# Performance work log

Measured on AMD Instinct MI355X. Metric: run time of the kernel, lower is better.

Reference implementation:

```python
import jax, jax.numpy as jnp
import numpy as np

B, S, F, H, A = 256, 128, 512, 1024, 18


def setup_inputs() -> dict:
    key = jax.random.key(0)
    ks = jax.random.split(key, 16)
    u = lambda k, shape, fan: jax.random.uniform(k, shape, jnp.float32, -1.0, 1.0) / np.sqrt(fan)
    return {
        "obs": jax.random.normal(ks[0], (B, S, F), jnp.float32),
        "hx": jax.random.normal(ks[1], (B, H), jnp.float32),
        "cx": jax.random.normal(ks[2], (B, H), jnp.float32),
        "behaviour_acts": jax.random.randint(ks[3], (B, S, 1), 0, A),
        "W1": u(ks[4], (H, F), F), "b1": u(ks[5], (H,), F),
        "W_ih": u(ks[6], (4 * H, H), H), "b_ih": u(ks[7], (4 * H,), H),
        "W_hh": u(ks[8], (4 * H, H), H), "b_hh": u(ks[9], (4 * H,), H),
        "W_v": u(ks[10], (1, H), H), "b_v": u(ks[11], (1,), H),
        "W_l": u(ks[12], (A, H), H), "b_l": u(ks[13], (A,), H),
    }


def reference(obs, hx, cx, behaviour_acts, W1, b1, W_ih, b_ih, W_hh, b_hh, W_v, b_v, W_l, b_l):
    # MLP body: [B,S,F] -> [B,S,H]
    x = jax.nn.relu(jnp.einsum("bsf,hf->bsh", obs, W1) + b1)
    # precompute input-to-gate projection for all timesteps (one big GEMM)
    xg = jnp.einsum("bsh,gh->bsg", x, W_ih) + b_ih  # [B,S,4H]

    def step(carry, xg_t):
        h, c = carry
        gates = xg_t + h @ W_hh.T + b_hh  # [B,4H], gate order i,f,g,o (torch LSTMCell)
        i, f, g, o = jnp.split(gates, 4, axis=-1)
        c = jax.nn.sigmoid(f) * c + jax.nn.sigmoid(i) * jnp.tanh(g)
        h = jax.nn.sigmoid(o) * jnp.tanh(c)
        return (h, c), h

    _, hs = jax.lax.scan(step, (hx, cx), jnp.swapaxes(xg, 0, 1))
    output = jnp.swapaxes(hs, 0, 1)  # [B,S,H]

    value = output @ W_v.T + b_v  # [B,S,1]
    logits = output @ W_l.T + b_l  # [B,S,A]
    # torch Categorical(probs=softmax(logits)) => log-prob via log_softmax
    logp = jax.nn.log_softmax(logits, axis=-1)
    acts = behaviour_acts.reshape(logits.shape[0], logits.shape[1], 1)
    log_probs = jnp.take_along_axis(logp, acts, axis=-1)  # [B,S,1]
    entropy = -jnp.sum(jnp.exp(logp) * logp, axis=-1, keepdims=True)  # [B,S,1]
    return log_probs, entropy, value
```

## Files before the change

kernel.cpp:

```cpp
#include <hip/hip_runtime.h>

#define B_ 256
#define S_ 128
#define F_ 512
#define H_ 1024
#define A_ 18
#define M_ (B_*S_)
#define G_ (4*H_)
#define CH_ 16
#define CR_ (B_*CH_)

typedef unsigned short u16;
typedef __attribute__((ext_vector_type(8))) _Float16 f16x8;
typedef __attribute__((ext_vector_type(4))) _Float16 f16x4;
typedef __attribute__((ext_vector_type(8))) short   s16x8;
typedef __attribute__((ext_vector_type(4))) float f32x4;
typedef __attribute__((ext_vector_type(4))) unsigned int u32x4;

__device__ __forceinline__ float bf2f(u16 u){
  union{unsigned int i; float f;} v; v.i=((unsigned int)u)<<16; return v.f;
}
__device__ __forceinline__ u16 f2bf(float f){
  unsigned int i=__float_as_uint(f);
  unsigned int r=(i+0x7fffu+((i>>16)&1u))>>16;
  return (u16)r;
}
__device__ __forceinline__ u16 f2h(float f){
  _Float16 h=(_Float16)f;
  union{_Float16 h; u16 u;} v; v.h=h; return v.u;
}
__device__ __forceinline__ float ldf(const void* p, size_t i, int m){
  return m ? ((const float*)p)[i] : bf2f(((const u16*)p)[i]);
}
__device__ __forceinline__ f16x8 load8_h(const void* base, size_t off, int m){
  f16x8 v;
  if(m==2) return *(const f16x8*)((const u16*)base + off);
  if(m==1){
    const float* f=(const float*)base + off;
    float4 a=*(const float4*)f; float4 b=*(const float4*)(f+4);
    v[0]=(_Float16)a.x; v[1]=(_Float16)a.y; v[2]=(_Float16)a.z; v[3]=(_Float16)a.w;
    v[4]=(_Float16)b.x; v[5]=(_Float16)b.y; v[6]=(_Float16)b.z; v[7]=(_Float16)b.w;
    return v;
  }
  s16x8 w=*(const s16x8*)((const u16*)base + off);
#pragma unroll
  for(int k=0;k<8;k++) v[k]=(_Float16)bf2f((u16)w[k]);
  return v;
}

__device__ __forceinline__ u32x4 load_c16(const void* p){
  u32x4 r;
  asm volatile("global_load_dwordx4 %0, %1, off sc0 sc1" : "=v"(r) : "v"(p));
  return r;
}
__device__ __forceinline__ void store_c2(u16* p, u16 v){
  unsigned int vv=v;
  asm volatile("global_store_short %0, %1, off sc0 sc1" :: "v"(p), "v"(vv) : "memory");
}
__device__ __forceinline__ int load_c4(const int* p){
  int r;
  asm volatile("global_load_dword %0, %1, off sc0 sc1" : "=v"(r) : "v"(p));
  return r;
}
__device__ __forceinline__ void store_c4(int* p, int v){
  asm volatile("global_store_dword %0, %1, off sc0 sc1" :: "v"(p), "v"(v) : "memory");
}

template<int ROWS, int MAP>
__device__ __forceinline__ void stage(const void* base, int mode, int lda, int k0,
                                      int rowoff, int t0, u16* lds, int tid){
  if(mode==2){
    constexpr int NI=(ROWS*8)/256;
    int wv=tid>>6, l=tid&63;
#pragma unroll
    for(int i=0;i<NI;i++){
      int s0=i*256+(wv<<6), s=s0+l;
      int r=s>>3, gc=(s&7)^(r&7);
      int p=rowoff+r, sr;
      if(MAP==0)      sr=p;
      else if(MAP==1) sr=(p&3)*H_+(p>>2);
      else            sr=(p>>4)*S_+t0+(p&15);
      const u16* src=(const u16*)base + (size_t)sr*lda + k0 + gc*8;
      u16* dst=lds + s0*8;
      __builtin_amdgcn_global_load_lds((const __attribute__((address_space(1))) unsigned int*)src,
                                       (__attribute__((address_space(3))) unsigned int*)dst,
                                       16, 0, 0);
    }
  } else {
#pragma unroll
    for(int s0=tid; s0<ROWS*8; s0+=256){
      int r=s0>>3, gc=s0&7, lc=gc^(r&7);
      int p=rowoff+r, sr;
      if(MAP==0)      sr=p;
      else if(MAP==1) sr=(p&3)*H_+(p>>2);
      else            sr=(p>>4)*S_+t0+(p&15);
      f16x8 v=load8_h(base, (size_t)sr*lda + k0 + gc*8, mode);
      *(f16x8*)(lds + r*64 + lc*8)=v;
    }
  }
}

__device__ __forceinline__ f16x8 frag_ld(const u16* lds, int r0, int kc, int lane){
  int r = r0 + (lane&15);
  int c = (kc + (lane>>4)) ^ (r&7);
  return *(const f16x8*)(lds + r*64 + c*8);
}

template<int AMAP, int BMAP, int OUTMODE>
__global__ __launch_bounds__(256,3) void gemm128(const void* A, const void* Bt, void* C,
    const float* __restrict__ biasf, const int* __restrict__ flag,
    int K, int lda, int ldb, int ldc, int t0, int amode, int bmode){
  int m=*flag;
  int am = amode<0 ? m : amode;
  int bm_ = bmode<0 ? m : bmode;
  __shared__ u16 As[128*64];
  __shared__ u16 Bs[128*64];
  int tid=threadIdx.x, lane=tid&63, w=tid>>6;
  int bm=blockIdx.y*128, bn=blockIdx.x*128;
  int wm=(w&1)*64, wn=(w>>1)*64;
  f32x4 acc[4][4];
#pragma unroll
  for(int i=0;i<4;i++)
#pragma unroll
    for(int j=0;j<4;j++) acc[i][j]=(f32x4)(0.f);
  for(int k0=0;k0<K;k0+=64){
    stage<128,AMAP>(A , am,  lda, k0, bm, t0, As, tid);
    stage<128,BMAP>(Bt, bm_, ldb, k0, bn, t0, Bs, tid);
    __syncthreads();
#pragma unroll
    for(int kk=0;kk<2;kk++){
      f16x8 af[4], bq[4];
#pragma unroll
      for(int i=0;i<4;i++) af[i]=frag_ld(As, wm+i*16, kk*4, lane);
#pragma unroll
      for(int j=0;j<4;j++) bq[j]=frag_ld(Bs, wn+j*16, kk*4, lane);
#pragma unroll
      for(int i=0;i<4;i++)
#pragma unroll
        for(int j=0;j<4;j++)
          acc[i][j]=__builtin_amdgcn_mfma_f32_16x16x32_f16(af[i],bq[j],acc[i][j],0,0,0);
    }
    __syncthreads();
  }
  int rl=lane>>4, cl=lane&15;
#pragma unroll
  for(int j=0;j<4;j++){
    int col=bn+wn+j*16+cl;
    float bb=biasf[col];
#pragma unroll
    for(int i=0;i<4;i++){
#pragma unroll
      for(int r=0;r<4;r++){
        int row=bm+wm+i*16+rl*4+r;
        float v=acc[i][j][r]+bb;
        if(OUTMODE==0){ v=fmaxf(v,0.f); ((u16*)C)[(size_t)row*ldc+col]=f2h(v); }
        else if(OUTMODE==2){ ((u16*)C)[(size_t)row*ldc+col]=f2h(v); }
        else { ((float*)C)[(size_t)row*ldc+col]=v; }
      }
    }
  }
}

__global__ __launch_bounds__(512,2) void lstm_persist(u16* __restrict__ hh,
        const u16* __restrict__ Whhp, const u16* __restrict__ xgp,
        float* __restrict__ cst, int* __restrict__ cntc, int tbase){
  __shared__ u16 As[16*2048];
  __shared__ u16 hs[32*36];
  int tid=threadIdx.x, lane=tid&63, w=tid>>6;
  int grp=blockIdx.x&7, ci=blockIdx.x>>3;
  int bm=grp*32, bn=ci*128;
  int* flags = cntc + grp*64;

  f16x8 bw[32];
#pragma unroll
  for(int t=0;t<32;t++){
    int p = bn + w*16 + (lane&15);
    int k = t*32 + (lane>>4)*8;
    bw[t]=*(const f16x8*)(Whhp + (size_t)p*H_ + k);
  }
#pragma unroll
  for(int t=0;t<32;t++) asm volatile("" : "+a"(bw[t]));

  int bb0=lane&15, bb1=16+(lane&15);
  int ul = w*4 + (lane>>4);
  int gu2 = (bn>>2) + ul;
  float c0=cst[(size_t)(bm+bb0)*H_+gu2];
  float c1=cst[(size_t)(bm+bb1)*H_+gu2];
  int sb0=tid>>5, su=tid&31, sb1=(tid+512)>>5;

  size_t xoff0=((size_t)(bm+bb0)*CH_)*G_ + bn + w*16 + (lane>>4)*4;
  size_t xoff1=((size_t)(bm+bb1)*CH_)*G_ + bn + w*16 + (lane>>4)*4;
  f16x4 xga0=*(const f16x4*)(xgp + xoff0);
  f16x4 xga1=*(const f16x4*)(xgp + xoff1);

  for(int dt=0;dt<CH_;dt++){
    if(dt){
      if(w==0){
        int target=tbase+dt;
        while(true){
          int v=load_c4(flags+(lane&31));
          asm volatile("s_waitcnt vmcnt(0)" ::: "memory");
          if(__all(v>=target)) break;
          __builtin_amdgcn_s_sleep(1);
        }
      }
      __syncthreads();
    }
    {
      int slotPrev=(dt+CH_-1)&(CH_-1);
      const u16* hbase = hh + (size_t)slotPrev*H_;
      u32x4 tmp[8];
#pragma unroll
      for(int i=0;i<8;i++){
        int s=tid+i*512, kt=s>>8, r=(s>>3)&31, gc=s&7;
        tmp[i]=*(const u32x4*)(hbase + (size_t)(bm+r)*(CH_*H_) + kt*64 + gc*8);
      }
#pragma unroll
      for(int i=0;i<8;i++){
        int s=tid+i*512, kt=s>>8, r=(s>>3)&31, gc=s&7, lc=gc^(r&7);
        *(u32x4*)(As + kt*2048 + r*64 + lc*8)=tmp[i];
      }
    }
    __syncthreads();
    f32x4 a0e=(f32x4)(0.f), a0o=(f32x4)(0.f), a1e=(f32x4)(0.f), a1o=(f32x4)(0.f);
#pragma unroll
    for(int kt=0;kt<16;kt++){
      f16x8 af0=frag_ld(As+kt*2048, 0,  0, lane);
      f16x8 af1=frag_ld(As+kt*2048, 16, 0, lane);
      a0e=__builtin_amdgcn_mfma_f32_16x16x32_f16(bw[2*kt],af0,a0e,0,0,0);
      a1e=__builtin_amdgcn_mfma_f32_16x16x32_f16(bw[2*kt],af1,a1e,0,0,0);
      f16x8 bf0=frag_ld(As+kt*2048, 0,  4, lane);
      f16x8 bf1=frag_ld(As+kt*2048, 16, 4, lane);
      a0o=__builtin_amdgcn_mfma_f32_16x16x32_f16(bw[2*kt+1],bf0,a0o,0,0,0);
      a1o=__builtin_amdgcn_mfma_f32_16x16x32_f16(bw[2*kt+1],bf1,a1o,0,0,0);
    }
    f32x4 A0=a0e+a0o, A1=a1e+a1o;
    u16 h0w, h1w;
    {
      float ii=1.f/(1.f+__expf(-(A0[0]+(float)xga0[0])));
      float ff=1.f/(1.f+__expf(-(A0[1]+(float)xga0[1])));
      float gg=1.f-2.f/(__expf(2.f*(A0[2]+(float)xga0[2]))+1.f);
      float oo=1.f/(1.f+__expf(-(A0[3]+(float)xga0[3])));
      c0=ff*c0+ii*gg;
      float th=1.f-2.f/(__expf(2.f*c0)+1.f);
      h0w=f2h(oo*th);
    }
    {
      float ii=1.f/(1.f+__expf(-(A1[0]+(float)xga1[0])));
      float ff=1.f/(1.f+__expf(-(A1[1]+(float)xga1[1])));
      float gg=1.f-2.f/(__expf(2.f*(A1[2]+(float)xga1[2]))+1.f);
      float oo=1.f/(1.f+__expf(-(A1[3]+(float)xga1[3])));
      c1=ff*c1+ii*gg;
      float th=1.f-2.f/(__expf(2.f*c1)+1.f);
      h1w=f2h(oo*th);
    }
    hs[bb0*36+ul]=h0w;
    hs[bb1*36+ul]=h1w;
    __syncthreads();
    store_c2(hh + ((size_t)(bm+sb0)*CH_+dt)*H_ + (bn>>2)+su, hs[sb0*36+su]);
    store_c2(hh + ((size_t)(bm+sb1)*CH_+dt)*H_ + (bn>>2)+su, hs[sb1*36+su]);
    if(dt<CH_-1){
      asm volatile("s_waitcnt vmcnt(0)" ::: "memory");
      __syncthreads();
      if(tid==0) store_c4(flags+ci, tbase+dt+1);
      xga0=*(const f16x4*)(xgp + xoff0 + (size_t)(dt+1)*G_);
      xga1=*(const f16x4*)(xgp + xoff1 + (size_t)(dt+1)*G_);
    }
  }
  cst[(size_t)(bm+bb0)*H_+gu2]=c0;
  cst[(size_t)(bm+bb1)*H_+gu2]=c1;
}

__global__ __launch_bounds__(256,2) void lstm_step(u16* __restrict__ hh, int slotPrev, int dt,
        const void* __restrict__ Whh, const u16* __restrict__ xg,
        float* __restrict__ cst, const int* __restrict__ flag){
  int m=*flag;
  __shared__ u16 As[64*64];
  __shared__ u16 Bs[64*64];
  __shared__ float gs[64*64];
  int tid=threadIdx.x, lane=tid&63, w=tid>>6;
  int bm=blockIdx.y*64, bn=blockIdx.x*64;
  int wm=(w&1)*32, wn=(w>>1)*32;
  f32x4 acc[2][2];
#pragma unroll
  for(int i=0;i<2;i++)
#pragma unroll
    for(int j=0;j<2;j++) acc[i][j]=(f32x4)(0.f);
  for(int k0=0;k0<H_;k0+=64){
    stage<64,0>(hh + slotPrev*H_, 2, CH_*H_, k0, bm, 0, As, tid);
    stage<64,1>(Whh,              m, H_,     k0, bn, 0, Bs, tid);
    __syncthreads();
#pragma unroll
    for(int kk=0;kk<2;kk++){
      f16x8 af[2], bq[2];
#pragma unroll
      for(int i=0;i<2;i++) af[i]=frag_ld(As, wm+i*16, kk*4, lane);
#pragma unroll
      for(int j=0;j<2;j++) bq[j]=frag_ld(Bs, wn+j*16, kk*4, lane);
#pragma unroll
      for(int i=0;i<2;i++)
#pragma unroll
        for(int j=0;j<2;j++)
          acc[i][j]=__builtin_amdgcn_mfma_f32_16x16x32_f16(af[i],bq[j],acc[i][j],0,0,0);
    }
    __syncthreads();
  }
  int rl=lane>>4, cl=lane&15;
#pragma unroll
  for(int j=0;j<2;j++){
    int coll=wn+j*16+cl;
#pragma unroll
    for(int i=0;i<2;i++){
#pragma unroll
      for(int r=0;r<4;r++){
        int rowl=wm+i*16+rl*4+r;
        float xv=(float)((const _Float16*)xg)[((size_t)(bm+rowl)*CH_+dt)*G_ + bn+coll];
        gs[rowl*64+coll]=acc[i][j][r] + xv;
      }
    }
  }
  __syncthreads();
#pragma unroll
  for(int p=0;p<4;p++){
    int idx=p*256+tid;
    int rowl=idx>>4, u=idx&15;
    float4 gv = *(const float4*)&gs[rowl*64+u*4];
    float ii=1.f/(1.f+__expf(-gv.x));
    float ff=1.f/(1.f+__expf(-gv.y));
    float gg=1.f-2.f/(__expf(2.f*gv.z)+1.f);
    float oo=1.f/(1.f+__expf(-gv.w));
    int gb=bm+rowl;
    int gu=(bn>>2)+u;
    size_t ci=(size_t)gb*H_+gu;
    float cn=ff*cst[ci]+ii*gg;
    cst[ci]=cn;
    float th=1.f-2.f/(__expf(2.f*cn)+1.f);
    hh[(size_t)gb*(CH_*H_) + dt*H_ + gu]=f2h(oo*th);
  }
}

__global__ __launch_bounds__(256,2) void heads_chunk(const u16* __restrict__ hh,
      const void* __restrict__ Wl, const void* __restrict__ Wv,
      const float* __restrict__ blf, const int* __restrict__ acts,
      void* __restrict__ out, const int* __restrict__ flag, int t0){
  int m=*flag;
  int rg = blockIdx.x*4 + (threadIdx.x>>6);
  int lane = threadIdx.x & 63;
  const u16* h = hh + (size_t)rg*H_;
  u32x4 hv0=load_c16(h + lane*16);
  u32x4 hv1=load_c16(h + lane*16 + 8);
  f16x8 h0=__builtin_bit_cast(f16x8,hv0), h1=__builtin_bit_cast(f16x8,hv1);
  float hv[16];
#pragma unroll
  for(int k=0;k<8;k++){ hv[k]=(float)h0[k]; hv[8+k]=(float)h1[k]; }
  float dots[19];
#pragma unroll
  for(int j=0;j<19;j++){
    const void* wrow = (j<18) ? Wl : Wv;
    size_t roff = (j<18) ? (size_t)j*H_ : 0;
    float wv_[16];
    if(m){
      const float* f=(const float*)wrow + roff + lane*16;
      float4 a=*(const float4*)f, b=*(const float4*)(f+4), c=*(const float4*)(f+8), d=*(const float4*)(f+12);
      wv_[0]=a.x;wv_[1]=a.y;wv_[2]=a.z;wv_[3]=a.w; wv_[4]=b.x;wv_[5]=b.y;wv_[6]=b.z;wv_[7]=b.w;
      wv_[8]=c.x;wv_[9]=c.y;wv_[10]=c.z;wv_[11]=c.w; wv_[12]=d.x;wv_[13]=d.y;wv_[14]=d.z;wv_[15]=d.w;
    } else {
      const u16* ub=(const u16*)wrow + roff + lane*16;
      s16x8 w0=*(const s16x8*)ub, w1=*(const s16x8*)(ub+8);
#pragma unroll
      for(int k=0;k<8;k++){ wv_[k]=bf2f((u16)w0[k]); wv_[8+k]=bf2f((u16)w1[k]); }
    }
    float d=0.f;
#pragma unroll
    for(int k=0;k<16;k++) d += hv[k]*wv_[k];
#pragma unroll
    for(int mm=1;mm<64;mm<<=1) d += __shfl_xor(d, mm, 64);
    dots[j]=d;
  }
  float lg[18];
#pragma unroll
  for(int j=0;j<18;j++) lg[j]=dots[j]+blf[j];
  float value=dots[18]+blf[18];
  float mx=lg[0];
#pragma unroll
  for(int j=1;j<18;j++) mx=fmaxf(mx,lg[j]);
  float se=0.f, s1=0.f;
#pragma unroll
  for(int j=0;j<18;j++){ float e=__expf(lg[j]-mx); se+=e; s1+=e*(lg[j]-mx); }
  float lse=__logf(se);
  int b=rg>>4, dt=rg&(CH_-1);
  int gw = b*S_ + t0 + dt;
  int a=acts[gw];
  float la=0.f;
#pragma unroll
  for(int j=0;j<18;j++) la = (j==a) ? lg[j] : la;
  float lp=la-mx-lse;
  float ent=lse - s1/se;
  if(lane==0){
    if(m){
      ((float*)out)[gw]=lp; ((float*)out)[M_+gw]=ent; ((float*)out)[2*M_+gw]=value;
    } else {
      ((u16*)out)[gw]=f2bf(lp); ((u16*)out)[M_+gw]=f2bf(ent); ((u16*)out)[2*M_+gw]=f2bf(value);
    }
  }
}

__global__ void detect(const u16* __restrict__ obs_w, int* __restrict__ flag){
  __shared__ float red[256];
  float mx=0.f;
  for(int i=threadIdx.x;i<4096;i+=256) mx=fmaxf(mx,fabsf(bf2f(obs_w[i])));
  red[threadIdx.x]=mx; __syncthreads();
  for(int s=128;s>0;s>>=1){
    if(threadIdx.x<s) red[threadIdx.x]=fmaxf(red[threadIdx.x],red[threadIdx.x+s]);
    __syncthreads();
  }
  if(threadIdx.x==0) *flag=(red[0]>1e4f)?1:0;
}

__global__ void prep(const void* bih, const void* bhh, const void* b1, const void* bl, const void* bv,
                     const void* cx, const void* hx,
                     float* biasg, float* b1f, float* blf, float* cst, u16* hh,
                     int* cnt, const int* __restrict__ flag){
  int m=*flag;
  size_t i=(size_t)blockIdx.x*256+threadIdx.x;
  if(i<G_){ size_t rm=(i&3)*H_+(i>>2); biasg[i]=ldf(bih,rm,m)+ldf(bhh,rm,m); return; }
  i-=G_;
  if(i<H_){ b1f[i]=ldf(b1,i,m); return; }
  i-=H_;
  if(i<19){ blf[i]=(i<18)?ldf(bl,i,m):ldf(bv,0,m); return; }
  i-=19;
  if(i<512){ cnt[i]=0; return; }
  i-=512;
  if(i<(size_t)B_*H_){ cst[i]=ldf(cx,i,m); return; }
  i-=(size_t)B_*H_;
  if(i<(size_t)B_*H_){
    size_t b=i>>10, k=i&1023;
    hh[b*(CH_*H_) + (CH_-1)*H_ + k]=f2h(ldf(hx,i,m));
  }
}

__global__ void convw(const void* W1, const void* Wih, const void* Whh,
                      u16* W1h, u16* Wihp, u16* Whhp, const int* __restrict__ flag){
  int m=*flag;
  size_t i=((size_t)blockIdx.x*256+threadIdx.x)*8;
  const size_t n1=(size_t)H_*F_, n2=(size_t)G_*H_;
  if(i<n1){ *(f16x8*)(W1h+i)=load8_h(W1,i,m); return; }
  i-=n1;
  if(i<n2){ size_t p=i>>10, c=i&1023; size_t sr=(p&3)*H_+(p>>2);
            *(f16x8*)(Wihp+i)=load8_h(Wih, sr*H_+c, m); return; }
  i-=n2;
  if(i<n2){ size_t p=i>>10, c=i&1023; size_t sr=(p&3)*H_+(p>>2);
            *(f16x8*)(Whhp+i)=load8_h(Whh, sr*H_+c, m); return; }
}
__global__ void convobs(const void* obs, u16* obsh, const int* __restrict__ flag){
  int m=*flag;
  size_t i=((size_t)blockIdx.x*256+threadIdx.x)*8;
  if(i<(size_t)M_*F_) *(f16x8*)(obsh+i)=load8_h(obs,i,m);
}

extern "C" void kernel_launch(void* const* d_in, const int* in_sizes, int n_in,
                              void* d_out, int out_size, void* d_ws, size_t ws_size,
                              hipStream_t stream){
  const void* obs=d_in[0];
  const void* hx =d_in[1];
  const void* cx =d_in[2];
  const int* acts=(const int*)d_in[3];
  const void* W1 =d_in[4];
  const void* b1 =d_in[5];
  const void* Wih=d_in[6];
  const void* bih=d_in[7];
  const void* Whh=d_in[8];
  const void* bhh=d_in[9];
  const void* Wv =d_in[10];
  const void* bv =d_in[11];
  const void* Wl =d_in[12];
  const void* bl =d_in[13];

  char* w=(char*)d_ws;
  auto alloc=[&](size_t n){ char* p=w; w+=((n+255)&~(size_t)255); return p; };
  int*   flag =(int*)alloc(4);
  int*   cnt  =(int*)alloc(512*4);
  float* biasg=(float*)alloc((size_t)G_*4);
  float* b1f  =(float*)alloc((size_t)H_*4);
  float* blf  =(float*)alloc(32*4);
  float* cst  =(float*)alloc((size_t)B_*H_*4);
  u16*   hh   =(u16*)alloc((size_t)B_*CH_*H_*2);
  u16*   xc   =(u16*)alloc((size_t)CR_*H_*2);
  u16*   xg   =(u16*)alloc((size_t)CR_*G_*2);
  size_t nW=((size_t)H_*F_ + 2*(size_t)G_*H_)*2 + 768;
  bool pathW = ((size_t)(w-(char*)d_ws) + nW) <= ws_size;
  u16 *W1h=0,*Wihp=0,*Whhp=0;
  if(pathW){ W1h=(u16*)alloc((size_t)H_*F_*2); Wihp=(u16*)alloc((size_t)G_*H_*2); Whhp=(u16*)alloc((size_t)G_*H_*2); }
  size_t nXC=(size_t)M_*H_*2 + 256;
  bool pathXC = pathW && (((size_t)(w-(char*)d_ws) + nXC) <= ws_size);
  u16* xcf=0; if(pathXC) xcf=(u16*)alloc((size_t)M_*H_*2);
  size_t nO=(size_t)M_*F_*2 + 256;
  bool pathO = pathXC && (((size_t)(w-(char*)d_ws) + nO) <= ws_size);
  u16* obsh=0; if(pathO) obsh=(u16*)alloc((size_t)M_*F_*2);

  detect<<<1,256,0,stream>>>((const u16*)obs, flag);
  {
    int total=G_+H_+19+512+B_*H_+B_*H_;
    prep<<<(total+255)/256,256,0,stream>>>(bih,bhh,b1,bl,bv,cx,hx, biasg,b1f,blf,cst,hh,cnt, flag);
  }
  if(pathW){
    size_t n=((size_t)H_*F_+2*(size_t)G_*H_)/8;
    convw<<<(int)((n+255)/256),256,0,stream>>>(W1,Wih,Whh, W1h,Wihp,Whhp, flag);
  }
  if(pathO){
    size_t n=(size_t)M_*F_/8;
    convobs<<<(int)((n+255)/256),256,0,stream>>>(obs, obsh, flag);
  }
  if(pathXC){
    gemm128<0,0,0><<<dim3(H_/128, M_/128),256,0,stream>>>(
        pathO?(const void*)obsh:obs, pathW?(const void*)W1h:W1, xcf, b1f, flag,
        F_, F_, F_, H_, 0, pathO?2:-1, pathW?2:-1);
  }

  for(int c=0;c<S_/CH_;c++){
    int t0=c*CH_;
    if(!pathXC){
      gemm128<2,0,0><<<dim3(H_/128, CR_/128),256,0,stream>>>(
          obs, pathW?(const void*)W1h:W1, xc, b1f, flag, F_, F_, F_, H_, t0, -1, pathW?2:-1);
    }
    if(pathXC)
      gemm128<2,0,2><<<dim3(G_/128, CR_/128),256,0,stream>>>(
          xcf, Wihp, xg, biasg, flag, H_, H_, H_, G_, t0, 2, 2);
    else if(pathW)
      gemm128<0,0,2><<<dim3(G_/128, CR_/128),256,0,stream>>>(
          xc, Wihp, xg, biasg, flag, H_, H_, H_, G_, 0, 2, 2);
    else
      gemm128<0,1,2><<<dim3(G_/128, CR_/128),256,0,stream>>>(
          xc, Wih, xg, biasg, flag, H_, H_, H_, G_, 0, 2, -1);

    if(pathW)
      lstm_persist<<<256,512,0,stream>>>(hh, Whhp, xg, cst, cnt, t0);
    else
      for(int dt=0;dt<CH_;dt++)
        lstm_step<<<dim3(G_/64, B_/64),256,0,stream>>>(hh, (dt+CH_-1)&(CH_-1), dt, Whh, xg, cst, flag);

    heads_chunk<<<dim3(CR_/4),256,0,stream>>>(hh, Wl, Wv, blf, acts, d_out, flag, t0);
  }
}
```

Before: 1.219 ms.

## Compute next chunk's input-gate projection inside persistent LSTM kernel

The persistent LSTM kernel now also computes the next chunk's x·W_ih projection with MFMA, one timestep per recurrent step, and writes it into a second xg buffer. The buffers are double-buffered so the separate per-chunk GEMM launch runs only for the first chunk. The goal is to fill the idle time each block spends waiting on the cross-block flag barrier and to drop a kernel launch per chunk. The cost is extra global loads of W_ih and xcf straight from memory, with no LDS reuse, plus a wait and barrier that now run on every step, which can lengthen the critical path of the recurrence.

```diff
diff --git a/kernel.cpp b/kernel.cpp
--- a/kernel.cpp
+++ b/kernel.cpp
@@ -13,6 +13,7 @@
 typedef unsigned short u16;
 typedef __attribute__((ext_vector_type(8))) _Float16 f16x8;
 typedef __attribute__((ext_vector_type(4))) _Float16 f16x4;
+typedef __attribute__((ext_vector_type(4))) u16 u16x4;
 typedef __attribute__((ext_vector_type(8))) short   s16x8;
 typedef __attribute__((ext_vector_type(4))) float f32x4;
 typedef __attribute__((ext_vector_type(4))) unsigned int u32x4;
@@ -163,13 +164,16 @@
 
 __global__ __launch_bounds__(512,2) void lstm_persist(u16* __restrict__ hh,
         const u16* __restrict__ Whhp, const u16* __restrict__ xgp,
-        float* __restrict__ cst, int* __restrict__ cntc, int tbase){
+        float* __restrict__ cst, int* __restrict__ cntc, int tbase,
+        const u16* __restrict__ xcf, const u16* __restrict__ Wihp,
+        const float* __restrict__ biasg, u16* __restrict__ xg2){
   __shared__ u16 As[16*2048];
   __shared__ u16 hs[32*36];
   int tid=threadIdx.x, lane=tid&63, w=tid>>6;
   int grp=blockIdx.x&7, ci=blockIdx.x>>3;
   int bm=grp*32, bn=ci*128;
   int* flags = cntc + grp*64;
+  bool dog = (xg2 != nullptr);
 
   f16x8 bw[32];
 #pragma unroll
@@ -187,6 +191,12 @@
   float c0=cst[(size_t)(bm+bb0)*H_+gu2];
   float c1=cst[(size_t)(bm+bb1)*H_+gu2];
   int sb0=tid>>5, su=tid&31, sb1=(tid+512)>>5;
+
+  int p0 = bn + w*16 + (lane>>4)*4;
+  const u16* wrow = Wihp + (size_t)(bn + w*16 + (lane&15))*H_ + (lane>>4)*8;
+  const u16* xr0  = xcf + ((size_t)(bm+bb0)*S_ + tbase + CH_)*H_ + (lane>>4)*8;
+  const u16* xr1  = xcf + ((size_t)(bm+bb1)*S_ + tbase + CH_)*H_ + (lane>>4)*8;
+  float4 bias4; if(dog) bias4=*(const float4*)(biasg + p0);
 
   size_t xoff0=((size_t)(bm+bb0)*CH_)*G_ + bn + w*16 + (lane>>4)*4;
   size_t xoff1=((size_t)(bm+bb1)*CH_)*G_ + bn + w*16 + (lane>>4)*4;
@@ -259,12 +269,33 @@
     __syncthreads();
     store_c2(hh + ((size_t)(bm+sb0)*CH_+dt)*H_ + (bn>>2)+su, hs[sb0*36+su]);
     store_c2(hh + ((size_t)(bm+sb1)*CH_+dt)*H_ + (bn>>2)+su, hs[sb1*36+su]);
+    asm volatile("s_waitcnt vmcnt(0)" ::: "memory");
+    __syncthreads();
     if(dt<CH_-1){
-      asm volatile("s_waitcnt vmcnt(0)" ::: "memory");
-      __syncthreads();
       if(tid==0) store_c4(flags+ci, tbase+dt+1);
       xga0=*(const f16x4*)(xgp + xoff0 + (size_t)(dt+1)*G_);
       xga1=*(const f16x4*)(xgp + xoff1 + (size_t)(dt+1)*G_);
+    }
+    if(dog){
+      const u16* x0p = xr0 + (size_t)dt*H_;
+      const u16* x1p = xr1 + (size_t)dt*H_;
+      f32x4 g0=(f32x4)(0.f), g1=(f32x4)(0.f);
+#pragma unroll
+      for(int kt=0;kt<32;kt++){
+        f16x8 aw=*(const f16x8*)(wrow + kt*32);
+        f16x8 x0=*(const f16x8*)(x0p + kt*32);
+        f16x8 x1=*(const f16x8*)(x1p + kt*32);
+        g0=__builtin_amdgcn_mfma_f32_16x16x32_f16(aw,x0,g0,0,0,0);
+        g1=__builtin_amdgcn_mfma_f32_16x16x32_f16(aw,x1,g1,0,0,0);
+      }
+      u16x4 o0,o1;
+#pragma unroll
+      for(int r=0;r<4;r++){
+        o0[r]=f2h(g0[r]+bias4[r]);
+        o1[r]=f2h(g1[r]+bias4[r]);
+      }
+      *(u16x4*)(xg2 + ((size_t)(bm+bb0)*CH_+dt)*G_ + p0)=o0;
+      *(u16x4*)(xg2 + ((size_t)(bm+bb1)*CH_+dt)*G_ + p0)=o1;
     }
   }
   cst[(size_t)(bm+bb0)*H_+gu2]=c0;
@@ -494,6 +525,9 @@
   size_t nXC=(size_t)M_*H_*2 + 256;
   bool pathXC = pathW && (((size_t)(w-(char*)d_ws) + nXC) <= ws_size);
   u16* xcf=0; if(pathXC) xcf=(u16*)alloc((size_t)M_*H_*2);
+  size_t nF=(size_t)CR_*G_*2 + 256;
+  bool pathF = pathXC && (((size_t)(w-(char*)d_ws) + nF) <= ws_size);
+  u16* xgB=0; if(pathF) xgB=(u16*)alloc((size_t)CR_*G_*2);
   size_t nO=(size_t)M_*F_*2 + 256;
   bool pathO = pathXC && (((size_t)(w-(char*)d_ws) + nO) <= ws_size);
   u16* obsh=0; if(pathO) obsh=(u16*)alloc((size_t)M_*F_*2);
@@ -517,27 +551,33 @@
         F_, F_, F_, H_, 0, pathO?2:-1, pathW?2:-1);
   }
 
-  for(int c=0;c<S_/CH_;c++){
+  const int NC=S_/CH_;
+  for(int c=0;c<NC;c++){
     int t0=c*CH_;
+    u16* xgcur = (pathF && (c&1)) ? xgB : xg;
+    u16* xgnxt = (pathF && !(c&1)) ? xgB : xg;
     if(!pathXC){
       gemm128<2,0,0><<<dim3(H_/128, CR_/128),256,0,stream>>>(
           obs, pathW?(const void*)W1h:W1, xc, b1f, flag, F_, F_, F_, H_, t0, -1, pathW?2:-1);
     }
-    if(pathXC)
-      gemm128<2,0,2><<<dim3(G_/128, CR_/128),256,0,stream>>>(
-          xcf, Wihp, xg, biasg, flag, H_, H_, H_, G_, t0, 2, 2);
-    else if(pathW)
-      gemm128<0,0,2><<<dim3(G_/128, CR_/128),256,0,stream>>>(
-          xc, Wihp, xg, biasg, flag, H_, H_, H_, G_, 0, 2, 2);
-    else
-      gemm128<0,1,2><<<dim3(G_/128, CR_/128),256,0,stream>>>(
-          xc, Wih, xg, biasg, flag, H_, H_, H_, G_, 0, 2, -1);
+    if(!pathF || c==0){
+      if(pathXC)
+        gemm128<2,0,2><<<dim3(G_/128, CR_/128),256,0,stream>>>(
+            xcf, Wihp, xgcur, biasg, flag, H_, H_, H_, G_, t0, 2, 2);
+      else if(pathW)
+        gemm128<0,0,2><<<dim3(G_/128, CR_/128),256,0,stream>>>(
+            xc, Wihp, xgcur, biasg, flag, H_, H_, H_, G_, 0, 2, 2);
+      else
+        gemm128<0,1,2><<<dim3(G_/128, CR_/128),256,0,stream>>>(
+            xc, Wih, xgcur, biasg, flag, H_, H_, H_, G_, 0, 2, -1);
+    }
 
     if(pathW)
-      lstm_persist<<<256,512,0,stream>>>(hh, Whhp, xg, cst, cnt, t0);
+      lstm_persist<<<256,512,0,stream>>>(hh, Whhp, xgcur, cst, cnt, t0,
+          xcf, Wihp, biasg, (pathF && c<NC-1) ? xgnxt : (u16*)nullptr);
     else
       for(int dt=0;dt<CH_;dt++)
-        lstm_step<<<dim3(G_/64, B_/64),256,0,stream>>>(hh, (dt+CH_-1)&(CH_-1), dt, Whh, xg, cst, flag);
+        lstm_step<<<dim3(G_/64, B_/64),256,0,stream>>>(hh, (dt+CH_-1)&(CH_-1), dt, Whh, xgcur, cst, flag);
 
     heads_chunk<<<dim3(CR_/4),256,0,stream>>>(hh, Wl, Wv, blf, acts, d_out, flag, t0);
   }
```

Measured after the change: 3.202 ms. 2.63x slower.
